# Kernel optimization log

Measured on AMD Instinct MI355X. Metric: run time of the kernel, lower is better.

The kernel has to match this reference:

```python
import jax, jax.numpy as jnp
import numpy as np

B, C, H, W = 8, 64, 64, 64
CQ = C // 2

def setup_inputs() -> dict:
    key = jax.random.key(0)
    ks = jax.random.split(key, 10)
    s = 0.05
    return {
        "x": jax.random.normal(ks[0], (B, C, H, W), jnp.float32),
        "wq": jax.random.normal(ks[1], (CQ, C), jnp.float32) * s,
        "bq": jax.random.normal(ks[2], (CQ,), jnp.float32) * s,
        "wk": jax.random.normal(ks[3], (CQ, C), jnp.float32) * s,
        "bk": jax.random.normal(ks[4], (CQ,), jnp.float32) * s,
        "wv": jax.random.normal(ks[5], (C, C), jnp.float32) * s,
        "bv": jax.random.normal(ks[6], (C,), jnp.float32) * s,
        "wf": jax.random.normal(ks[7], (C, C), jnp.float32) * s,
        "bf": jax.random.normal(ks[8], (C,), jnp.float32) * s,
        "gamma": jnp.ones((1,), jnp.float32),
    }

def _conv1x1(w, b, x):
    # 1x1 conv == channel matmul: [O,C] x [B,C,H,W] -> [B,O,H,W]
    return jnp.einsum('oc,bchw->bohw', w, x) + b[None, :, None, None]

def reference(x, wq, bq, wk, bk, wv, bv, wf, bf, gamma):
    b, c, h, w = x.shape
    n = h * w
    q = _conv1x1(wq, bq, x).reshape(b, -1, n)   # [B, C/2, N]
    k = _conv1x1(wk, bk, x).reshape(b, -1, n)   # [B, C/2, N]
    v = _conv1x1(wv, bv, x).reshape(b, c, n)    # [B, C,   N]
    scale = 1.0 / jnp.sqrt(jnp.float32(n))
    energy = jnp.einsum('bcn,bcm->bnm', q, k) * scale  # [B, N, N]
    attn = jax.nn.softmax(energy, axis=-1)
    out = jnp.einsum('bcm,bnm->bcn', v, attn)          # V @ attn^T
    out = out.reshape(b, c, h, w)
    out = _conv1x1(wf, bf, out)
    return gamma[0] * out + x
```

## Files before the change

### kernel.cpp

```cpp
#include <hip/hip_runtime.h>

typedef unsigned short u16;
typedef unsigned int   u32;
typedef __bf16  bf16x8 __attribute__((ext_vector_type(8)));
typedef float   f32x16 __attribute__((ext_vector_type(16)));
typedef u32     u32x4  __attribute__((ext_vector_type(4)));

#define NN  4096
#define CCH 64
#define CQ  32
#define K1S 0.0225421092623961f

__device__ __forceinline__ u16 bfc(float a) { return __builtin_bit_cast(u16, (__bf16)a); }

__device__ __forceinline__ u32 e2pk(float a, float b) {
  float ea, eb; u32 r;
  asm("v_exp_f32 %0, %1" : "=v"(ea) : "v"(a));
  asm("v_exp_f32 %0, %1" : "=v"(eb) : "v"(b));
  asm("v_cvt_pk_bf16_f32 %0, %1, %2" : "=v"(r) : "v"(ea), "v"(eb));
  return r;
}

__device__ __forceinline__ void gload16(const void* g, void* l) {
  __builtin_amdgcn_global_load_lds((const __attribute__((address_space(1))) void*)g,
                                   (__attribute__((address_space(3))) void*)l, 16, 0, 0);
}


__global__ __launch_bounds__(512) void qkv_kernel(
    const float* __restrict__ x,
    const float* __restrict__ wq, const float* __restrict__ bq,
    const float* __restrict__ wk, const float* __restrict__ bk,
    const float* __restrict__ wv, const float* __restrict__ bv,
    u16* __restrict__ qT, char* __restrict__ kws, char* __restrict__ vws)
{
  __shared__ float xs[64][64];
  __shared__ u16 qls[64][34];
  __shared__ u16 kls[64][34];
  __shared__ u16 vls[64][66];
  const int bid = blockIdx.x;
  const int b = bid >> 6;
  const int chunk = bid & 63;
  const int nbase = chunk * 64;
  const int t = threadIdx.x, lane = t & 63, wid = t >> 6;

  {
    const float* xb = x + (size_t)b * CCH * NN + nbase;
    const int row = t >> 3, colq = (t & 7) * 2;
    float4 v0 = *(const float4*)(xb + (size_t)row * NN + colq * 4);
    float4 v1 = *(const float4*)(xb + (size_t)row * NN + colq * 4 + 4);
    float4* dst = (float4*)&xs[0][0];
    dst[row * 16 + colq]     = v0;
    dst[row * 16 + colq + 1] = v1;
  }
  __syncthreads();

  float xcol[64];
  #pragma unroll
  for (int c = 0; c < 64; ++c) xcol[c] = xs[c][lane];

  const float* w; const float* bias; float sc = 1.0f;
  const int sub = (wid & 1) * 16;
  if (wid < 2)      { w = wq + sub * 64; bias = bq + sub; sc = K1S; }
  else if (wid < 4) { w = wk + sub * 64; bias = bk + sub; }
  else              { w = wv + (wid - 4) * 16 * 64; bias = bv + (wid - 4) * 16; }

  #pragma unroll 2
  for (int i = 0; i < 16; ++i) {
    float a = bias[i];
    #pragma unroll
    for (int c = 0; c < 64; ++c) a = fmaf(w[i * 64 + c], xcol[c], a);
    a *= sc;
    u16 hv = bfc(a);
    if (wid < 2)      qls[lane][sub + i] = hv;
    else if (wid < 4) kls[lane][sub + i] = hv;
    else              vls[(wid - 4) * 16 + i][lane] = hv;
  }
  __syncthreads();

  u32* qdst = (u32*)(qT + ((size_t)b * NN + nbase) * CQ);
  #pragma unroll
  for (int jj = 0; jj < 2; ++jj) {
    int i = t + 512 * jj;
    int n = i >> 4, cp = i & 15;
    qdst[i] = *(const u32*)&qls[n][cp * 2];
  }
  u32* kimg = (u32*)(kws + ((size_t)b * 64 + chunk) * 4096);
  #pragma unroll
  for (int jj = 0; jj < 2; ++jj) {
    int i = t + 512 * jj;
    int reg = i >> 8, l = (i >> 2) & 63, j2 = i & 3;
    int s = reg >> 1, ks = reg & 1;
    int key = s * 32 + (l & 31);
    int ck  = ks * 16 + (l >> 5) * 8 + j2 * 2;
    kimg[i] = *(const u32*)&kls[key][ck];
  }
  u32* vimg = (u32*)(vws + ((size_t)b * 64 + chunk) * 8192);
  #pragma unroll
  for (int jj = 0; jj < 4; ++jj) {
    int i = t + 512 * jj;
    int reg = i >> 8, l = (i >> 2) & 63, j2 = i & 3;
    int s = reg >> 2, kb = (reg >> 1) & 1, ct = reg & 1;
    int c   = ct * 32 + (l & 31);
    int key = s * 32 + kb * 16 + (l >> 5) * 4 + (j2 >> 1) * 8 + (j2 & 1) * 2;
    vimg[i] = *(const u32*)&vls[c][key];
  }
}

template<int NSPLIT>
__global__ __launch_bounds__(256, 2) void attn_kernel(
    const u16* __restrict__ qT, const char* __restrict__ kws, const char* __restrict__ vws,
    u32* __restrict__ opart, float* __restrict__ lpart)
{
  constexpr int CH = 64 / NSPLIT;
  __shared__ __align__(16) char kbuf[3][4096];
  __shared__ __align__(16) char vbuf[3][8192];
  const int bid = blockIdx.x;
  const int b = bid & 7, qt = (bid >> 3) & 15, split = bid >> 7;
  const int t = threadIdx.x, lane = t & 63, wid = t >> 6;
  const int h = lane >> 5, c31 = lane & 31;

  const u16* qpA = qT + ((size_t)b * NN + qt * 256 + wid * 64 + c31) * CQ + h * 8;
  const bf16x8 qfA0 = *(const bf16x8*)(qpA);
  const bf16x8 qfA1 = *(const bf16x8*)(qpA + 16);
  const bf16x8 qfB0 = *(const bf16x8*)(qpA + 32 * CQ);
  const bf16x8 qfB1 = *(const bf16x8*)(qpA + 32 * CQ + 16);

  const char* ksrc = kws + ((size_t)b * 64 + split * CH) * 4096 + t * 16;
  const char* vsrc = vws + ((size_t)b * 64 + split * CH) * 8192 + t * 16;

  auto stage = [&](int buf, int it) {
    gload16(ksrc + (size_t)it * 4096, &kbuf[buf][wid * 1024]);
    gload16(vsrc + (size_t)it * 8192, &vbuf[buf][wid * 1024]);
    gload16(vsrc + (size_t)it * 8192 + 4096, &vbuf[buf][4096 + wid * 1024]);
  };

  const bf16x8 onef = __builtin_bit_cast(bf16x8,
      (u32x4){0x3F803F80u, 0x3F803F80u, 0x3F803F80u, 0x3F803F80u});

  f32x16 accA0 = {}, accA1 = {}, accB0 = {}, accB1 = {}, laccA = {}, laccB = {};
  const int lofs = lane * 16;

  stage(0, 0);
  stage(1, 1);

  #pragma unroll
  for (int it = 0; it < CH; ++it) {
    if (it == CH - 1) asm volatile("s_waitcnt vmcnt(0)" ::: "memory");
    else              asm volatile("s_waitcnt vmcnt(3)" ::: "memory");
    __builtin_amdgcn_s_barrier();
    __builtin_amdgcn_sched_barrier(0);
    if (it + 2 < CH) stage((it + 2) % 3, it + 2);
    const int cur = it % 3;

    const bf16x8 kf0 = *(const bf16x8*)&kbuf[cur][lofs];
    const bf16x8 kf1 = *(const bf16x8*)&kbuf[cur][1024 + lofs];
    const bf16x8 kf2 = *(const bf16x8*)&kbuf[cur][2048 + lofs];
    const bf16x8 kf3 = *(const bf16x8*)&kbuf[cur][3072 + lofs];

    f32x16 sA0, sA1, sB0, sB1;
    __builtin_amdgcn_s_setprio(1);
    sA0 = __builtin_amdgcn_mfma_f32_32x32x16_bf16(kf0, qfA0, (f32x16){}, 0, 0, 0);
    sA0 = __builtin_amdgcn_mfma_f32_32x32x16_bf16(kf1, qfA1, sA0, 0, 0, 0);
    sA1 = __builtin_amdgcn_mfma_f32_32x32x16_bf16(kf2, qfA0, (f32x16){}, 0, 0, 0);
    sA1 = __builtin_amdgcn_mfma_f32_32x32x16_bf16(kf3, qfA1, sA1, 0, 0, 0);
    sB0 = __builtin_amdgcn_mfma_f32_32x32x16_bf16(kf0, qfB0, (f32x16){}, 0, 0, 0);
    sB0 = __builtin_amdgcn_mfma_f32_32x32x16_bf16(kf1, qfB1, sB0, 0, 0, 0);
    sB1 = __builtin_amdgcn_mfma_f32_32x32x16_bf16(kf2, qfB0, (f32x16){}, 0, 0, 0);
    sB1 = __builtin_amdgcn_mfma_f32_32x32x16_bf16(kf3, qfB1, sB1, 0, 0, 0);
    __builtin_amdgcn_s_setprio(0);

    u32 pwA[16] __attribute__((aligned(16)));
    u32 pwB[16] __attribute__((aligned(16)));
    #pragma unroll
    for (int r = 0; r < 16; r += 2) {
      pwA[r >> 1]       = e2pk(sA0[r], sA0[r + 1]);
      pwA[8 + (r >> 1)] = e2pk(sA1[r], sA1[r + 1]);
      pwB[r >> 1]       = e2pk(sB0[r], sB0[r + 1]);
      pwB[8 + (r >> 1)] = e2pk(sB1[r], sB1[r + 1]);
    }

    __builtin_amdgcn_s_setprio(1);
    #pragma unroll
    for (int s = 0; s < 2; ++s) {
      #pragma unroll
      for (int kb = 0; kb < 2; ++kb) {
        const bf16x8 pfA = __builtin_bit_cast(bf16x8, *(const u32x4*)&pwA[s * 8 + kb * 4]);
        const bf16x8 pfB = __builtin_bit_cast(bf16x8, *(const u32x4*)&pwB[s * 8 + kb * 4]);
        const bf16x8 vf0 = *(const bf16x8*)&vbuf[cur][(s * 4 + kb * 2) * 1024 + lofs];
        const bf16x8 vf1 = *(const bf16x8*)&vbuf[cur][(s * 4 + kb * 2 + 1) * 1024 + lofs];
        accA0 = __builtin_amdgcn_mfma_f32_32x32x16_bf16(vf0, pfA, accA0, 0, 0, 0);
        accA1 = __builtin_amdgcn_mfma_f32_32x32x16_bf16(vf1, pfA, accA1, 0, 0, 0);
        accB0 = __builtin_amdgcn_mfma_f32_32x32x16_bf16(vf0, pfB, accB0, 0, 0, 0);
        accB1 = __builtin_amdgcn_mfma_f32_32x32x16_bf16(vf1, pfB, accB1, 0, 0, 0);
        laccA = __builtin_amdgcn_mfma_f32_32x32x16_bf16(onef, pfA, laccA, 0, 0, 0);
        laccB = __builtin_amdgcn_mfma_f32_32x32x16_bf16(onef, pfB, laccB, 0, 0, 0);
      }
    }
    __builtin_amdgcn_s_setprio(0);
  }

  const int qt128 = qt * 2 + (wid >> 1);
  const size_t obase = ((size_t)(b * 32 + qt128) * NSPLIT + split) * 4096;
  #pragma unroll
  for (int j = 0; j < 2; ++j) {
    const int col = (wid & 1) * 64 + j * 32 + c31;
    #pragma unroll
    for (int ct = 0; ct < 2; ++ct) {
      const f32x16& a = j ? (ct ? accB1 : accB0) : (ct ? accA1 : accA0);
      #pragma unroll
      for (int g2 = 0; g2 < 4; ++g2) {
        #pragma unroll
        for (int b2 = 0; b2 < 2; ++b2) {
          int cp = ct * 16 + g2 * 4 + h * 2 + b2;
          float lo = a[g2 * 4 + b2 * 2], hi = a[g2 * 4 + b2 * 2 + 1];
          u32 pr; asm("v_cvt_pk_bf16_f32 %0, %1, %2" : "=v"(pr) : "v"(lo), "v"(hi));
          opart[obase + cp * 128 + col] = pr;
        }
      }
    }
    if (h == 0) {
      const f32x16& l = j ? laccB : laccA;
      lpart[((size_t)(b * 32 + qt128) * NSPLIT + split) * 128 + col] = l[0];
    }
  }
}

template<int NSPLIT>
__global__ __launch_bounds__(512) void combine_kernel(
    const u32* __restrict__ opart, const float* __restrict__ lpart,
    const float* __restrict__ x, const float* __restrict__ wf, const float* __restrict__ bfb,
    const float* __restrict__ gamma, float* __restrict__ out)
{
  __shared__ float ols[64][65];
  __shared__ float linv[64];
  const int bid = blockIdx.x;
  const int b = bid & 7, qt64 = bid >> 3;
  const int qt128 = qt64 >> 1, qh = qt64 & 1;
  const int t = threadIdx.x, lane = t & 63, wid = t >> 6;

  const u32* ob = opart + (size_t)(b * 32 + qt128) * NSPLIT * 4096 + qh * 64;
  #pragma unroll
  for (int jj = 0; jj < 4; ++jj) {
    int i = t + 512 * jj;
    int cp = i >> 6, q = i & 63;
    float lo = 0.f, hi = 0.f;
    #pragma unroll
    for (int s = 0; s < NSPLIT; ++s) {
      u32 a = ob[s * 4096 + cp * 128 + q];
      lo += __builtin_bit_cast(float, (a << 16));
      hi += __builtin_bit_cast(float, (a & 0xffff0000u));
    }
    ols[cp * 2][q]     = lo;
    ols[cp * 2 + 1][q] = hi;
  }
  if (t < 64) {
    const float* lp = lpart + (size_t)(b * 32 + qt128) * NSPLIT * 128 + qh * 64;
    float l = 0.f;
    #pragma unroll
    for (int s = 0; s < NSPLIT; ++s) l += lp[s * 128 + t];
    linv[t] = 1.f / l;
  }
  __syncthreads();

  const float oinv = linv[lane];
  float oc[64];
  #pragma unroll
  for (int c = 0; c < 64; ++c) oc[c] = ols[c][lane] * oinv;
  const float gm = gamma[0];
  const size_t nidx = (size_t)qt64 * 64 + lane;
  #pragma unroll
  for (int i = 0; i < 8; ++i) {
    const int o = wid * 8 + i;
    float a = bfb[o];
    #pragma unroll
    for (int c = 0; c < 64; ++c) a = fmaf(wf[o * 64 + c], oc[c], a);
    const size_t idx = ((size_t)b * CCH + o) * NN + nidx;
    out[idx] = gm * a + x[idx];
  }
}

extern "C" void kernel_launch(void* const* d_in, const int* in_sizes, int n_in,
                              void* d_out, int out_size, void* d_ws, size_t ws_size,
                              hipStream_t stream) {
  const float* x     = (const float*)d_in[0];
  const float* wq    = (const float*)d_in[1];
  const float* bq    = (const float*)d_in[2];
  const float* wk    = (const float*)d_in[3];
  const float* bk    = (const float*)d_in[4];
  const float* wv    = (const float*)d_in[5];
  const float* bv    = (const float*)d_in[6];
  const float* wf    = (const float*)d_in[7];
  const float* bf_   = (const float*)d_in[8];
  const float* gamma = (const float*)d_in[9];
  float* out = (float*)d_out;

  u16* qT   = (u16*)d_ws;
  char* kws = (char*)(qT + (size_t)8 * NN * CQ);
  char* vws = kws + (size_t)8 * 64 * 4096;
  u32* opart = (u32*)(vws + (size_t)8 * 64 * 8192);
  const size_t base = 2097152ull + 2097152ull + 4194304ull;
  const size_t need4 = base + 4ull * (4194304ull + 131072ull);

  qkv_kernel<<<dim3(512), dim3(512), 0, stream>>>(x, wq, bq, wk, bk, wv, bv, qT, kws, vws);
  if (ws_size >= need4) {
    float* lpart = (float*)(opart + (size_t)8 * 32 * 4 * 4096);
    attn_kernel<4><<<dim3(512), dim3(256), 0, stream>>>(qT, kws, vws, opart, lpart);
    combine_kernel<4><<<dim3(512), dim3(512), 0, stream>>>(opart, lpart, x, wf, bf_, gamma, out);
  } else {
    float* lpart = (float*)(opart + (size_t)8 * 32 * 2 * 4096);
    attn_kernel<2><<<dim3(256), dim3(256), 0, stream>>>(qT, kws, vws, opart, lpart);
    combine_kernel<2><<<dim3(512), dim3(512), 0, stream>>>(opart, lpart, x, wf, bf_, gamma, out);
  }
}
```

Baseline: 90.02 us.

## Halve per-wave query tile, add 8-way key split, sum softmax denominator in VALU

Each attention wave now handles 32 queries instead of 64, and the key dimension is split 8 ways when the workspace allows. Together these quadruple the grid to 2048 blocks and allow 3 blocks per CU, with LDS staging cut from triple to double buffering. The row-sum of exp values is now accumulated with scalar adds plus a cross-half shuffle, replacing the MFMA-with-ones trick. The qkv kernel's block-to-batch mapping is also interleaved. The cost is that K/V tiles are reloaded twice as often per query, prefetch depth drops, and combine must read more partials.

```diff
diff --git a/kernel.cpp b/kernel.cpp
--- a/kernel.cpp
+++ b/kernel.cpp
@@ -13,10 +13,11 @@
 
 __device__ __forceinline__ u16 bfc(float a) { return __builtin_bit_cast(u16, (__bf16)a); }
 
-__device__ __forceinline__ u32 e2pk(float a, float b) {
+__device__ __forceinline__ u32 e2pk_s(float a, float b, float& ps) {
   float ea, eb; u32 r;
   asm("v_exp_f32 %0, %1" : "=v"(ea) : "v"(a));
   asm("v_exp_f32 %0, %1" : "=v"(eb) : "v"(b));
+  ps += ea + eb;
   asm("v_cvt_pk_bf16_f32 %0, %1, %2" : "=v"(r) : "v"(ea), "v"(eb));
   return r;
 }
@@ -39,8 +40,8 @@
   __shared__ u16 kls[64][34];
   __shared__ u16 vls[64][66];
   const int bid = blockIdx.x;
-  const int b = bid >> 6;
-  const int chunk = bid & 63;
+  const int b = bid & 7;
+  const int chunk = bid >> 3;
   const int nbase = chunk * 64;
   const int t = threadIdx.x, lane = t & 63, wid = t >> 6;
 
@@ -108,23 +109,21 @@
 }
 
 template<int NSPLIT>
-__global__ __launch_bounds__(256, 2) void attn_kernel(
+__global__ __launch_bounds__(256, 3) void attn_kernel(
     const u16* __restrict__ qT, const char* __restrict__ kws, const char* __restrict__ vws,
     u32* __restrict__ opart, float* __restrict__ lpart)
 {
   constexpr int CH = 64 / NSPLIT;
-  __shared__ __align__(16) char kbuf[3][4096];
-  __shared__ __align__(16) char vbuf[3][8192];
+  __shared__ __align__(16) char kbuf[2][4096];
+  __shared__ __align__(16) char vbuf[2][8192];
   const int bid = blockIdx.x;
-  const int b = bid & 7, qt = (bid >> 3) & 15, split = bid >> 7;
+  const int b = bid & 7, qt128 = (bid >> 3) & 31, split = bid >> 8;
   const int t = threadIdx.x, lane = t & 63, wid = t >> 6;
   const int h = lane >> 5, c31 = lane & 31;
 
-  const u16* qpA = qT + ((size_t)b * NN + qt * 256 + wid * 64 + c31) * CQ + h * 8;
-  const bf16x8 qfA0 = *(const bf16x8*)(qpA);
-  const bf16x8 qfA1 = *(const bf16x8*)(qpA + 16);
-  const bf16x8 qfB0 = *(const bf16x8*)(qpA + 32 * CQ);
-  const bf16x8 qfB1 = *(const bf16x8*)(qpA + 32 * CQ + 16);
+  const u16* qp = qT + ((size_t)b * NN + qt128 * 128 + wid * 32 + c31) * CQ + h * 8;
+  const bf16x8 qf0 = *(const bf16x8*)(qp);
+  const bf16x8 qf1 = *(const bf16x8*)(qp + 16);
 
   const char* ksrc = kws + ((size_t)b * 64 + split * CH) * 4096 + t * 16;
   const char* vsrc = vws + ((size_t)b * 64 + split * CH) * 8192 + t * 16;
@@ -135,95 +134,76 @@
     gload16(vsrc + (size_t)it * 8192 + 4096, &vbuf[buf][4096 + wid * 1024]);
   };
 
-  const bf16x8 onef = __builtin_bit_cast(bf16x8,
-      (u32x4){0x3F803F80u, 0x3F803F80u, 0x3F803F80u, 0x3F803F80u});
-
-  f32x16 accA0 = {}, accA1 = {}, accB0 = {}, accB1 = {}, laccA = {}, laccB = {};
+  f32x16 acc0 = {}, acc1 = {};
+  float lsum = 0.f;
   const int lofs = lane * 16;
 
   stage(0, 0);
-  stage(1, 1);
 
   #pragma unroll
   for (int it = 0; it < CH; ++it) {
-    if (it == CH - 1) asm volatile("s_waitcnt vmcnt(0)" ::: "memory");
-    else              asm volatile("s_waitcnt vmcnt(3)" ::: "memory");
+    asm volatile("s_waitcnt vmcnt(0)" ::: "memory");
     __builtin_amdgcn_s_barrier();
     __builtin_amdgcn_sched_barrier(0);
-    if (it + 2 < CH) stage((it + 2) % 3, it + 2);
-    const int cur = it % 3;
+    if (it + 1 < CH) stage((it + 1) & 1, it + 1);
+    const int cur = it & 1;
 
     const bf16x8 kf0 = *(const bf16x8*)&kbuf[cur][lofs];
     const bf16x8 kf1 = *(const bf16x8*)&kbuf[cur][1024 + lofs];
     const bf16x8 kf2 = *(const bf16x8*)&kbuf[cur][2048 + lofs];
     const bf16x8 kf3 = *(const bf16x8*)&kbuf[cur][3072 + lofs];
 
-    f32x16 sA0, sA1, sB0, sB1;
+    u32 pw[16] __attribute__((aligned(16)));
+    {
+      f32x16 s0, s1;
+      __builtin_amdgcn_s_setprio(1);
+      s0 = __builtin_amdgcn_mfma_f32_32x32x16_bf16(kf0, qf0, (f32x16){}, 0, 0, 0);
+      s0 = __builtin_amdgcn_mfma_f32_32x32x16_bf16(kf1, qf1, s0, 0, 0, 0);
+      s1 = __builtin_amdgcn_mfma_f32_32x32x16_bf16(kf2, qf0, (f32x16){}, 0, 0, 0);
+      s1 = __builtin_amdgcn_mfma_f32_32x32x16_bf16(kf3, qf1, s1, 0, 0, 0);
+      __builtin_amdgcn_s_setprio(0);
+      #pragma unroll
+      for (int r = 0; r < 16; r += 2) {
+        pw[r >> 1]       = e2pk_s(s0[r], s0[r + 1], lsum);
+        pw[8 + (r >> 1)] = e2pk_s(s1[r], s1[r + 1], lsum);
+      }
+    }
+
     __builtin_amdgcn_s_setprio(1);
-    sA0 = __builtin_amdgcn_mfma_f32_32x32x16_bf16(kf0, qfA0, (f32x16){}, 0, 0, 0);
-    sA0 = __builtin_amdgcn_mfma_f32_32x32x16_bf16(kf1, qfA1, sA0, 0, 0, 0);
-    sA1 = __builtin_amdgcn_mfma_f32_32x32x16_bf16(kf2, qfA0, (f32x16){}, 0, 0, 0);
-    sA1 = __builtin_amdgcn_mfma_f32_32x32x16_bf16(kf3, qfA1, sA1, 0, 0, 0);
-    sB0 = __builtin_amdgcn_mfma_f32_32x32x16_bf16(kf0, qfB0, (f32x16){}, 0, 0, 0);
-    sB0 = __builtin_amdgcn_mfma_f32_32x32x16_bf16(kf1, qfB1, sB0, 0, 0, 0);
-    sB1 = __builtin_amdgcn_mfma_f32_32x32x16_bf16(kf2, qfB0, (f32x16){}, 0, 0, 0);
-    sB1 = __builtin_amdgcn_mfma_f32_32x32x16_bf16(kf3, qfB1, sB1, 0, 0, 0);
-    __builtin_amdgcn_s_setprio(0);
-
-    u32 pwA[16] __attribute__((aligned(16)));
-    u32 pwB[16] __attribute__((aligned(16)));
-    #pragma unroll
-    for (int r = 0; r < 16; r += 2) {
-      pwA[r >> 1]       = e2pk(sA0[r], sA0[r + 1]);
-      pwA[8 + (r >> 1)] = e2pk(sA1[r], sA1[r + 1]);
-      pwB[r >> 1]       = e2pk(sB0[r], sB0[r + 1]);
-      pwB[8 + (r >> 1)] = e2pk(sB1[r], sB1[r + 1]);
-    }
-
-    __builtin_amdgcn_s_setprio(1);
-    #pragma unroll
-    for (int s = 0; s < 2; ++s) {
+    #pragma unroll
+    for (int s2 = 0; s2 < 2; ++s2) {
       #pragma unroll
-      for (int kb = 0; kb < 2; ++kb) {
-        const bf16x8 pfA = __builtin_bit_cast(bf16x8, *(const u32x4*)&pwA[s * 8 + kb * 4]);
-        const bf16x8 pfB = __builtin_bit_cast(bf16x8, *(const u32x4*)&pwB[s * 8 + kb * 4]);
-        const bf16x8 vf0 = *(const bf16x8*)&vbuf[cur][(s * 4 + kb * 2) * 1024 + lofs];
-        const bf16x8 vf1 = *(const bf16x8*)&vbuf[cur][(s * 4 + kb * 2 + 1) * 1024 + lofs];
-        accA0 = __builtin_amdgcn_mfma_f32_32x32x16_bf16(vf0, pfA, accA0, 0, 0, 0);
-        accA1 = __builtin_amdgcn_mfma_f32_32x32x16_bf16(vf1, pfA, accA1, 0, 0, 0);
-        accB0 = __builtin_amdgcn_mfma_f32_32x32x16_bf16(vf0, pfB, accB0, 0, 0, 0);
-        accB1 = __builtin_amdgcn_mfma_f32_32x32x16_bf16(vf1, pfB, accB1, 0, 0, 0);
-        laccA = __builtin_amdgcn_mfma_f32_32x32x16_bf16(onef, pfA, laccA, 0, 0, 0);
-        laccB = __builtin_amdgcn_mfma_f32_32x32x16_bf16(onef, pfB, laccB, 0, 0, 0);
+      for (int kb2 = 0; kb2 < 2; ++kb2) {
+        const bf16x8 pf = __builtin_bit_cast(bf16x8, *(const u32x4*)&pw[s2 * 8 + kb2 * 4]);
+        const bf16x8 vf0 = *(const bf16x8*)&vbuf[cur][(s2 * 4 + kb2 * 2) * 1024 + lofs];
+        const bf16x8 vf1 = *(const bf16x8*)&vbuf[cur][(s2 * 4 + kb2 * 2 + 1) * 1024 + lofs];
+        acc0 = __builtin_amdgcn_mfma_f32_32x32x16_bf16(vf0, pf, acc0, 0, 0, 0);
+        acc1 = __builtin_amdgcn_mfma_f32_32x32x16_bf16(vf1, pf, acc1, 0, 0, 0);
       }
     }
     __builtin_amdgcn_s_setprio(0);
   }
 
-  const int qt128 = qt * 2 + (wid >> 1);
+  lsum += __shfl_xor(lsum, 32, 64);
+
   const size_t obase = ((size_t)(b * 32 + qt128) * NSPLIT + split) * 4096;
-  #pragma unroll
-  for (int j = 0; j < 2; ++j) {
-    const int col = (wid & 1) * 64 + j * 32 + c31;
-    #pragma unroll
-    for (int ct = 0; ct < 2; ++ct) {
-      const f32x16& a = j ? (ct ? accB1 : accB0) : (ct ? accA1 : accA0);
+  const int col = wid * 32 + c31;
+  #pragma unroll
+  for (int ct = 0; ct < 2; ++ct) {
+    const f32x16& a = ct ? acc1 : acc0;
+    #pragma unroll
+    for (int g2 = 0; g2 < 4; ++g2) {
       #pragma unroll
-      for (int g2 = 0; g2 < 4; ++g2) {
-        #pragma unroll
-        for (int b2 = 0; b2 < 2; ++b2) {
-          int cp = ct * 16 + g2 * 4 + h * 2 + b2;
-          float lo = a[g2 * 4 + b2 * 2], hi = a[g2 * 4 + b2 * 2 + 1];
-          u32 pr; asm("v_cvt_pk_bf16_f32 %0, %1, %2" : "=v"(pr) : "v"(lo), "v"(hi));
-          opart[obase + cp * 128 + col] = pr;
-        }
+      for (int b2 = 0; b2 < 2; ++b2) {
+        int cp = ct * 16 + g2 * 4 + h * 2 + b2;
+        float lo = a[g2 * 4 + b2 * 2], hi = a[g2 * 4 + b2 * 2 + 1];
+        u32 pr; asm("v_cvt_pk_bf16_f32 %0, %1, %2" : "=v"(pr) : "v"(lo), "v"(hi));
+        opart[obase + cp * 128 + col] = pr;
       }
     }
-    if (h == 0) {
-      const f32x16& l = j ? laccB : laccA;
-      lpart[((size_t)(b * 32 + qt128) * NSPLIT + split) * 128 + col] = l[0];
-    }
-  }
+  }
+  if (h == 0)
+    lpart[((size_t)(b * 32 + qt128) * NSPLIT + split) * 128 + col] = lsum;
 }
 
 template<int NSPLIT>
@@ -300,16 +280,21 @@
   char* vws = kws + (size_t)8 * 64 * 4096;
   u32* opart = (u32*)(vws + (size_t)8 * 64 * 8192);
   const size_t base = 2097152ull + 2097152ull + 4194304ull;
+  const size_t need8 = base + 8ull * (4194304ull + 131072ull);
   const size_t need4 = base + 4ull * (4194304ull + 131072ull);
 
   qkv_kernel<<<dim3(512), dim3(512), 0, stream>>>(x, wq, bq, wk, bk, wv, bv, qT, kws, vws);
-  if (ws_size >= need4) {
+  if (ws_size >= need8) {
+    float* lpart = (float*)(opart + (size_t)8 * 32 * 8 * 4096);
+    attn_kernel<8><<<dim3(2048), dim3(256), 0, stream>>>(qT, kws, vws, opart, lpart);
+    combine_kernel<8><<<dim3(512), dim3(512), 0, stream>>>(opart, lpart, x, wf, bf_, gamma, out);
+  } else if (ws_size >= need4) {
     float* lpart = (float*)(opart + (size_t)8 * 32 * 4 * 4096);
-    attn_kernel<4><<<dim3(512), dim3(256), 0, stream>>>(qT, kws, vws, opart, lpart);
+    attn_kernel<4><<<dim3(1024), dim3(256), 0, stream>>>(qT, kws, vws, opart, lpart);
     combine_kernel<4><<<dim3(512), dim3(512), 0, stream>>>(opart, lpart, x, wf, bf_, gamma, out);
   } else {
     float* lpart = (float*)(opart + (size_t)8 * 32 * 2 * 4096);
-    attn_kernel<2><<<dim3(256), dim3(256), 0, stream>>>(qT, kws, vws, opart, lpart);
+    attn_kernel<2><<<dim3(512), dim3(256), 0, stream>>>(qT, kws, vws, opart, lpart);
     combine_kernel<2><<<dim3(512), dim3(512), 0, stream>>>(opart, lpart, x, wf, bf_, gamma, out);
   }
 }
```

New measurement: 95.61 us. 1.06x slower.
